# Kernel tuning notes

Hardware: AMD Instinct MI355X
Metric: run time of the kernel (lower is better)

## Reference

```python
import jax, jax.numpy as jnp
import numpy as np

RNN_SIZE = 2048
ATT_HID = 512


def setup_inputs() -> dict:
    key = jax.random.key(0)
    k1, k2, k3, k4, k5, k6, k7 = jax.random.split(key, 7)
    B, L = 128, 196
    h = jax.random.normal(k1, (B, RNN_SIZE), dtype=jnp.float32)
    att_feats = jax.random.normal(k2, (B, L, RNN_SIZE), dtype=jnp.float32)
    internal_att_feats = jax.random.normal(k3, (B, L, ATT_HID), dtype=jnp.float32)
    s = 1.0 / np.sqrt(RNN_SIZE)
    h2att_w = jax.random.uniform(k4, (ATT_HID, RNN_SIZE), jnp.float32, -s, s)
    h2att_b = jax.random.uniform(k5, (ATT_HID,), jnp.float32, -s, s)
    s2 = 1.0 / np.sqrt(ATT_HID)
    alpha_w = jax.random.uniform(k6, (1, ATT_HID), jnp.float32, -s2, s2)
    alpha_b = jax.random.uniform(k7, (1,), jnp.float32, -s2, s2)
    return {"h": h, "att_feats": att_feats, "internal_att_feats": internal_att_feats,
            "h2att_w": h2att_w, "h2att_b": h2att_b, "alpha_w": alpha_w, "alpha_b": alpha_b}


def reference(h, att_feats, internal_att_feats, h2att_w, h2att_b, alpha_w, alpha_b):
    # att_h: [B, att_hid] -> broadcast over att_size L
    att_h = h @ h2att_w.T + h2att_b                      # [B, A]
    dot = jnp.tanh(internal_att_feats + att_h[:, None, :])  # [B, L, A]
    scores = jnp.einsum('bla,a->bl', dot, alpha_w[0]) + alpha_b[0]  # [B, L]
    weight = jax.nn.softmax(scores, axis=1)              # [B, L]
    att_res = jnp.einsum('bl,bld->bd', weight, att_feats)  # [B, rnn_size]
    return att_res
```

## Files before the change

### kernel.cpp

```cpp
#include <hip/hip_runtime.h>

#define RNN 2048
#define AH  512
#define BB  128
#define LL  196

__device__ __forceinline__ float tanh_fast(float x) {
    float e = __expf(2.0f * x);
    return 1.0f - 2.0f * __builtin_amdgcn_rcpf(e + 1.0f);
}

__global__ __launch_bounds__(256) void k1_atth(const float* __restrict__ h,
                                               const float* __restrict__ w,
                                               const float* __restrict__ bias,
                                               float* __restrict__ att_h) {
    __shared__ float hs[4 * RNN];
    const int tid  = threadIdx.x;
    const int wv   = tid >> 6, lane = tid & 63;
    const int b0   = blockIdx.y * 4;
    const int a0   = blockIdx.x * 32 + wv * 8;

    const float4* hg  = reinterpret_cast<const float4*>(h + (size_t)b0 * RNN);
    float4*       hs4 = reinterpret_cast<float4*>(hs);
    #pragma unroll
    for (int i = 0; i < 8; ++i) hs4[tid + i * 256] = hg[tid + i * 256];
    __syncthreads();

    float acc[8][4];
    #pragma unroll
    for (int ai = 0; ai < 8; ++ai)
        #pragma unroll
        for (int bl = 0; bl < 4; ++bl) acc[ai][bl] = 0.f;

    const float4* w4 = reinterpret_cast<const float4*>(w);
    #pragma unroll 1
    for (int i = 0; i < 8; ++i) {
        const int k4 = i * 64 + lane;
        float4 hv[4];
        #pragma unroll
        for (int bl = 0; bl < 4; ++bl) hv[bl] = hs4[bl * 512 + k4];
        #pragma unroll
        for (int ai = 0; ai < 8; ++ai) {
            float4 wvv = w4[(size_t)(a0 + ai) * 512 + k4];
            #pragma unroll
            for (int bl = 0; bl < 4; ++bl)
                acc[ai][bl] += wvv.x * hv[bl].x + wvv.y * hv[bl].y
                             + wvv.z * hv[bl].z + wvv.w * hv[bl].w;
        }
    }

    #pragma unroll
    for (int off = 32; off; off >>= 1)
        #pragma unroll
        for (int ai = 0; ai < 8; ++ai)
            #pragma unroll
            for (int bl = 0; bl < 4; ++bl)
                acc[ai][bl] += __shfl_xor(acc[ai][bl], off);

    if (lane == 0) {
        #pragma unroll
        for (int ai = 0; ai < 8; ++ai) {
            const float ba = bias[a0 + ai];
            #pragma unroll
            for (int bl = 0; bl < 4; ++bl)
                att_h[(b0 + bl) * AH + a0 + ai] = acc[ai][bl] + ba;
        }
    }
}

__global__ __launch_bounds__(512) void k2_scores(const float* __restrict__ iaf,
                                                 const float* __restrict__ att_h,
                                                 const float* __restrict__ aw,
                                                 const float* __restrict__ ab,
                                                 float* __restrict__ scores) {
    const int wid  = blockIdx.x * 8 + (threadIdx.x >> 6);
    const int lane = threadIdx.x & 63;
    if (wid >= BB * LL) return;
    const int b = wid / LL, l = wid - b * LL;

    const float4* ir = reinterpret_cast<const float4*>(iaf + (size_t)(b * LL + l) * AH);
    const float4* hr = reinterpret_cast<const float4*>(att_h + (size_t)b * AH);
    const float4* ar = reinterpret_cast<const float4*>(aw);

    float s = 0.f;
    #pragma unroll
    for (int c = 0; c < 2; ++c) {
        int idx = lane + c * 64;
        float4 iv = ir[idx];
        float4 hv = hr[idx];
        float4 av = ar[idx];
        s += tanh_fast(iv.x + hv.x) * av.x
           + tanh_fast(iv.y + hv.y) * av.y
           + tanh_fast(iv.z + hv.z) * av.z
           + tanh_fast(iv.w + hv.w) * av.w;
    }
    #pragma unroll
    for (int off = 32; off; off >>= 1) s += __shfl_xor(s, off);
    if (lane == 0) scores[b * LL + l] = s + ab[0];
}

__global__ __launch_bounds__(512) void k4_out(const float* __restrict__ af,
                                              const float* __restrict__ scores,
                                              float* __restrict__ out) {
    const int b  = blockIdx.y;
    const int t  = threadIdx.x;
    const int lg = t >> 7;
    const int tt = t & 127;
    const int d0 = blockIdx.x * 512 + tt * 4;

    __shared__ float  wsm[LL];
    __shared__ float  red[8];
    __shared__ float4 p4[4][128];

    float v0 = (t < LL) ? scores[b * LL + t] : -1e30f;
    float m = v0;
    #pragma unroll
    for (int off = 32; off; off >>= 1) m = fmaxf(m, __shfl_xor(m, off));
    if ((t & 63) == 0) red[t >> 6] = m;
    __syncthreads();
    m = fmaxf(fmaxf(fmaxf(red[0], red[1]), fmaxf(red[2], red[3])),
              fmaxf(fmaxf(red[4], red[5]), fmaxf(red[6], red[7])));
    __syncthreads();

    float e0 = (t < LL) ? __expf(v0 - m) : 0.f;
    float s = e0;
    #pragma unroll
    for (int off = 32; off; off >>= 1) s += __shfl_xor(s, off);
    if ((t & 63) == 0) red[t >> 6] = s;
    __syncthreads();
    s = red[0] + red[1] + red[2] + red[3] + red[4] + red[5] + red[6] + red[7];
    const float inv = 1.f / s;
    if (t < LL) wsm[t] = e0 * inv;
    __syncthreads();

    const float* base = af + (size_t)b * LL * RNN + d0 + (size_t)(lg * 49) * RNN;
    float4 acc = {0.f, 0.f, 0.f, 0.f};
    #pragma unroll 7
    for (int i = 0; i < 49; ++i) {
        float wl = wsm[lg * 49 + i];
        float4 v = *reinterpret_cast<const float4*>(base + (size_t)i * RNN);
        acc.x += wl * v.x; acc.y += wl * v.y; acc.z += wl * v.z; acc.w += wl * v.w;
    }
    p4[lg][tt] = acc;
    __syncthreads();

    if (lg == 0) {
        float4 a0 = p4[0][tt], a1 = p4[1][tt], a2 = p4[2][tt], a3 = p4[3][tt];
        float4 r;
        r.x = (a0.x + a1.x) + (a2.x + a3.x);
        r.y = (a0.y + a1.y) + (a2.y + a3.y);
        r.z = (a0.z + a1.z) + (a2.z + a3.z);
        r.w = (a0.w + a1.w) + (a2.w + a3.w);
        *reinterpret_cast<float4*>(out + (size_t)b * RNN + d0) = r;
    }
}

extern "C" void kernel_launch(void* const* d_in, const int* in_sizes, int n_in,
                              void* d_out, int out_size, void* d_ws, size_t ws_size,
                              hipStream_t stream) {
    const float* h    = (const float*)d_in[0];
    const float* af   = (const float*)d_in[1];
    const float* iaf  = (const float*)d_in[2];
    const float* w    = (const float*)d_in[3];
    const float* bias = (const float*)d_in[4];
    const float* aw   = (const float*)d_in[5];
    const float* ab   = (const float*)d_in[6];
    float* out = (float*)d_out;

    float* ws_f    = (float*)d_ws;
    float* att_h   = ws_f;
    float* scores  = ws_f + BB * AH;

    k1_atth<<<dim3(16, 32), 256, 0, stream>>>(h, w, bias, att_h);

    int nwl = BB * LL;
    k2_scores<<<(nwl + 7) / 8, 512, 0, stream>>>(iaf, att_h, aw, ab, scores);

    k4_out<<<dim3(4, BB), 512, 0, stream>>>(af, scores, out);
}
```

Measured before the change: 59.29 us.

## Fuse three attention kernels into one cooperative kernel with grid syncs

Merges the att_h GEMV, the tanh score pass and the softmax-weighted reduction into a single persistent cooperative kernel of 512 blocks, with grid.sync between phases. This removes two kernel launch boundaries and their drain and refill gaps. In exchange, every phase runs on a fixed 512x512 grid: the score phase loops over work items and the GEMV uses smaller per-wave tiles. Grid-wide barriers add their own cost, and the original three-launch path is kept as a fallback if the cooperative launch fails.

```diff
diff --git a/kernel.cpp b/kernel.cpp
--- a/kernel.cpp
+++ b/kernel.cpp
@@ -1,4 +1,7 @@
 #include <hip/hip_runtime.h>
+#include <hip/hip_cooperative_groups.h>
+
+namespace cg = cooperative_groups;
 
 #define RNN 2048
 #define AH  512
@@ -8,6 +11,163 @@
 __device__ __forceinline__ float tanh_fast(float x) {
     float e = __expf(2.0f * x);
     return 1.0f - 2.0f * __builtin_amdgcn_rcpf(e + 1.0f);
+}
+
+__global__ __launch_bounds__(512, 4) void mega(const float* __restrict__ h,
+                                               const float* __restrict__ af,
+                                               const float* __restrict__ iaf,
+                                               const float* __restrict__ w,
+                                               const float* __restrict__ bias,
+                                               const float* __restrict__ aw,
+                                               const float* __restrict__ ab,
+                                               float* __restrict__ att_h,
+                                               float* __restrict__ scores,
+                                               float* __restrict__ out) {
+    __shared__ __align__(16) float smem[4 * RNN];
+    cg::grid_group grid = cg::this_grid();
+
+    const int tid  = threadIdx.x;
+    const int wv   = tid >> 6, lane = tid & 63;
+
+    {
+        const int bx = blockIdx.x & 15;
+        const int by = blockIdx.x >> 4;
+        const int b0 = by * 4;
+        const int a0 = bx * 32 + wv * 4;
+
+        const float4* hg  = reinterpret_cast<const float4*>(h + (size_t)b0 * RNN);
+        float4*       hs4 = reinterpret_cast<float4*>(smem);
+        #pragma unroll
+        for (int i = 0; i < 4; ++i) hs4[tid + i * 512] = hg[tid + i * 512];
+        __syncthreads();
+
+        float acc[4][4];
+        #pragma unroll
+        for (int ai = 0; ai < 4; ++ai)
+            #pragma unroll
+            for (int bl = 0; bl < 4; ++bl) acc[ai][bl] = 0.f;
+
+        const float4* w4 = reinterpret_cast<const float4*>(w);
+        #pragma unroll 1
+        for (int i = 0; i < 8; ++i) {
+            const int k4 = i * 64 + lane;
+            float4 hv[4];
+            #pragma unroll
+            for (int bl = 0; bl < 4; ++bl) hv[bl] = hs4[bl * 512 + k4];
+            #pragma unroll
+            for (int ai = 0; ai < 4; ++ai) {
+                float4 wvv = w4[(size_t)(a0 + ai) * 512 + k4];
+                #pragma unroll
+                for (int bl = 0; bl < 4; ++bl)
+                    acc[ai][bl] += wvv.x * hv[bl].x + wvv.y * hv[bl].y
+                                 + wvv.z * hv[bl].z + wvv.w * hv[bl].w;
+            }
+        }
+
+        #pragma unroll
+        for (int off = 32; off; off >>= 1)
+            #pragma unroll
+            for (int ai = 0; ai < 4; ++ai)
+                #pragma unroll
+                for (int bl = 0; bl < 4; ++bl)
+                    acc[ai][bl] += __shfl_xor(acc[ai][bl], off);
+
+        if (lane == 0) {
+            #pragma unroll
+            for (int ai = 0; ai < 4; ++ai) {
+                const float ba = bias[a0 + ai];
+                #pragma unroll
+                for (int bl = 0; bl < 4; ++bl)
+                    att_h[(size_t)(b0 + bl) * AH + a0 + ai] = acc[ai][bl] + ba;
+            }
+        }
+        __syncthreads();
+    }
+
+    grid.sync();
+
+    {
+        const int wid0 = blockIdx.x * 8 + wv;
+        const float4* ar = reinterpret_cast<const float4*>(aw);
+        for (int wid = wid0; wid < BB * LL; wid += 4096) {
+            const int b = wid / LL, l = wid - b * LL;
+            const float4* ir = reinterpret_cast<const float4*>(iaf + (size_t)(b * LL + l) * AH);
+            const float4* hr = reinterpret_cast<const float4*>(att_h + (size_t)b * AH);
+            float s = 0.f;
+            #pragma unroll
+            for (int c = 0; c < 2; ++c) {
+                int idx = lane + c * 64;
+                float4 iv = ir[idx];
+                float4 hv = hr[idx];
+                float4 av = ar[idx];
+                s += tanh_fast(iv.x + hv.x) * av.x
+                   + tanh_fast(iv.y + hv.y) * av.y
+                   + tanh_fast(iv.z + hv.z) * av.z
+                   + tanh_fast(iv.w + hv.w) * av.w;
+            }
+            #pragma unroll
+            for (int off = 32; off; off >>= 1) s += __shfl_xor(s, off);
+            if (lane == 0) scores[b * LL + l] = s + ab[0];
+        }
+    }
+
+    grid.sync();
+
+    {
+        float* wsm = smem;
+        float* red = smem + 224;
+        float4* p4 = reinterpret_cast<float4*>(smem + 256);
+
+        const int b  = blockIdx.x >> 2;
+        const int dc = blockIdx.x & 3;
+        const int t  = tid;
+        const int lg = t >> 7;
+        const int tt = t & 127;
+        const int d0 = dc * 512 + tt * 4;
+
+        float v0 = (t < LL) ? scores[b * LL + t] : -1e30f;
+        float m = v0;
+        #pragma unroll
+        for (int off = 32; off; off >>= 1) m = fmaxf(m, __shfl_xor(m, off));
+        if ((t & 63) == 0) red[t >> 6] = m;
+        __syncthreads();
+        m = fmaxf(fmaxf(fmaxf(red[0], red[1]), fmaxf(red[2], red[3])),
+                  fmaxf(fmaxf(red[4], red[5]), fmaxf(red[6], red[7])));
+        __syncthreads();
+
+        float e0 = (t < LL) ? __expf(v0 - m) : 0.f;
+        float s = e0;
+        #pragma unroll
+        for (int off = 32; off; off >>= 1) s += __shfl_xor(s, off);
+        if ((t & 63) == 0) red[t >> 6] = s;
+        __syncthreads();
+        s = red[0] + red[1] + red[2] + red[3] + red[4] + red[5] + red[6] + red[7];
+        const float inv = 1.f / s;
+        if (t < LL) wsm[t] = e0 * inv;
+        __syncthreads();
+
+        const float* base = af + (size_t)b * LL * RNN + d0 + (size_t)(lg * 49) * RNN;
+        float4 acc = {0.f, 0.f, 0.f, 0.f};
+        #pragma unroll 7
+        for (int i = 0; i < 49; ++i) {
+            float wl = wsm[lg * 49 + i];
+            float4 v = *reinterpret_cast<const float4*>(base + (size_t)i * RNN);
+            acc.x += wl * v.x; acc.y += wl * v.y; acc.z += wl * v.z; acc.w += wl * v.w;
+        }
+        p4[lg * 128 + tt] = acc;
+        __syncthreads();
+
+        if (lg == 0) {
+            float4 a0 = p4[0 * 128 + tt], a1 = p4[1 * 128 + tt];
+            float4 a2 = p4[2 * 128 + tt], a3 = p4[3 * 128 + tt];
+            float4 r;
+            r.x = (a0.x + a1.x) + (a2.x + a3.x);
+            r.y = (a0.y + a1.y) + (a2.y + a3.y);
+            r.z = (a0.z + a1.z) + (a2.z + a3.z);
+            r.w = (a0.w + a1.w) + (a2.w + a3.w);
+            *reinterpret_cast<float4*>(out + (size_t)b * RNN + d0) = r;
+        }
+    }
 }
 
 __global__ __launch_bounds__(256) void k1_atth(const float* __restrict__ h,
@@ -48,7 +208,6 @@
                              + wvv.z * hv[bl].z + wvv.w * hv[bl].w;
         }
     }
-
     #pragma unroll
     for (int off = 32; off; off >>= 1)
         #pragma unroll
@@ -167,14 +326,18 @@
     const float* ab   = (const float*)d_in[6];
     float* out = (float*)d_out;
 
-    float* ws_f    = (float*)d_ws;
-    float* att_h   = ws_f;
-    float* scores  = ws_f + BB * AH;
-
-    k1_atth<<<dim3(16, 32), 256, 0, stream>>>(h, w, bias, att_h);
-
-    int nwl = BB * LL;
-    k2_scores<<<(nwl + 7) / 8, 512, 0, stream>>>(iaf, att_h, aw, ab, scores);
-
-    k4_out<<<dim3(4, BB), 512, 0, stream>>>(af, scores, out);
-}
+    float* ws_f   = (float*)d_ws;
+    float* att_h  = ws_f;
+    float* scores = ws_f + BB * AH;
+
+    void* args[] = {(void*)&h, (void*)&af, (void*)&iaf, (void*)&w, (void*)&bias,
+                    (void*)&aw, (void*)&ab, (void*)&att_h, (void*)&scores, (void*)&out};
+    hipError_t err = hipLaunchCooperativeKernel((const void*)mega, dim3(512), dim3(512),
+                                                args, 0, stream);
+    if (err != hipSuccess) {
+        k1_atth<<<dim3(16, 32), 256, 0, stream>>>(h, w, bias, att_h);
+        int nwl = BB * LL;
+        k2_scores<<<(nwl + 7) / 8, 512, 0, stream>>>(iaf, att_h, aw, ab, scores);
+        k4_out<<<dim3(4, BB), 512, 0, stream>>>(af, scores, out);
+    }
+}
```

Measured after the change: 171.7 us. 190% more time.
